# Performance work log

Measured on AMD Instinct MI355X. Metric: run time of the kernel, lower is better.

Reference implementation:

```python
import jax, jax.numpy as jnp
import numpy as np

N = 50000       # nodes
E = 800000      # edges (avg degree 16)
DIN = 64        # input feature dim
HID = 128       # hidden dim (= per-head out_channels in GATConv)
HEADS = 4
G = 64          # graphs in the batch
NC = 8          # num classes
EPS = 1e-5      # BatchNorm eps
NEG_SLOPE = 0.2 # GAT leaky_relu slope


def setup_inputs():
    key = jax.random.key(0)
    it = iter(jax.random.split(key, 40))
    def p(shape, s=0.05):
        return jax.random.normal(next(it), shape, jnp.float32) * s
    x = jax.random.normal(next(it), (N, DIN), jnp.float32)
    edge_index = jax.random.randint(next(it), (2, E), 0, N)
    batch = jnp.sort(jax.random.randint(next(it), (N,), 0, G))
    inp = dict(x=x, edge_index=edge_index, batch=batch)
    inp["s0_Wl"] = p((DIN, HID)); inp["s0_Wr"] = p((DIN, HID)); inp["s0_b"] = p((HID,))
    inp["s1_Wl"] = p((HID, HID)); inp["s1_Wr"] = p((HID, HID)); inp["s1_b"] = p((HID,))
    inp["bn_g"] = 1.0 + p((4, HID)); inp["bn_b"] = p((4, HID))
    inp["bn_m"] = p((4, HID)); inp["bn_v"] = 0.5 + jax.random.uniform(next(it), (4, HID))
    inp["prelu_a"] = 0.25 + p((4, HID))
    for i in range(2):
        inp[f"g{i}_W"] = p((HID, HEADS * HID))
        inp[f"g{i}_as"] = p((HEADS, HID)); inp[f"g{i}_ad"] = p((HEADS, HID))
        inp[f"g{i}_bias"] = p((HID,))
    inp["idp_W"] = p((3, HID, HID)); inp["idp_b"] = p((3, HID)); inp["idp_a"] = 0.25 + p((2, HID))
    inp["cls_W"] = p((HID, NC)); inp["cls_b"] = p((NC,))
    return inp


def _bn(x, g, b, m, v):
    return (x - m) * jax.lax.rsqrt(v + EPS) * g + b


def _prelu(x, a):
    return jnp.where(x >= 0, x, a * x)


def _sage(x, src, dst, Wl, Wr, b):
    # PyG SAGEConv: lin_l(mean_{j->i} x_j) + lin_r(x_i)
    s = jax.ops.segment_sum(x[src], dst, num_segments=N)
    cnt = jax.ops.segment_sum(jnp.ones((src.shape[0],), x.dtype), dst, num_segments=N)
    agg = s / jnp.maximum(cnt, 1.0)[:, None]
    return agg @ Wl + b + x @ Wr


def _gat(x, src, dst, W, a_src, a_dst, bias):
    # src/dst already include self-loops (PyG GATConv default). concat=False -> mean over heads.
    xw = (x @ W).reshape(N, HEADS, HID)               # [N,H,C]
    es = jnp.einsum('nhc,hc->nh', xw, a_src)          # [N,H]
    ed = jnp.einsum('nhc,hc->nh', xw, a_dst)
    e = jax.nn.leaky_relu(es[src] + ed[dst], NEG_SLOPE)   # [E2,H]
    m = jax.lax.stop_gradient(jax.ops.segment_max(e, dst, num_segments=N))
    ex = jnp.exp(e - m[dst])
    den = jax.ops.segment_sum(ex, dst, num_segments=N)
    alpha = ex / den[dst]                                  # [E2,H] softmax per destination
    # per-head scatter to keep peak memory ~[E2,C] instead of [E2,H,C]
    heads = [jax.ops.segment_sum(alpha[:, h:h + 1] * xw[src, h, :], dst, num_segments=N)
             for h in range(HEADS)]
    return jnp.stack(heads, 1).mean(1) + bias


def _model(x, edge_index, batch, s0_Wl, s0_Wr, s0_b, s1_Wl, s1_Wr, s1_b,
           bn_g, bn_b, bn_m, bn_v, prelu_a,
           g0_W, g0_as, g0_ad, g0_bias, g1_W, g1_as, g1_ad, g1_bias,
           idp_W, idp_b, idp_a, cls_W, cls_b):
    src, dst = edge_index[0], edge_index[1]
    h = _sage(x, src, dst, s0_Wl, s0_Wr, s0_b)
    h = _prelu(_bn(h, bn_g[0], bn_b[0], bn_m[0], bn_v[0]), prelu_a[0])
    h = _sage(h, src, dst, s1_Wl, s1_Wr, s1_b)
    h = _prelu(_bn(h, bn_g[1], bn_b[1], bn_m[1], bn_v[1]), prelu_a[1])
    loop = jnp.arange(N)
    src2 = jnp.concatenate([src, loop]); dst2 = jnp.concatenate([dst, loop])
    h = _gat(h, src2, dst2, g0_W, g0_as, g0_ad, g0_bias)
    h = _prelu(_bn(h, bn_g[2], bn_b[2], bn_m[2], bn_v[2]), prelu_a[2])
    h = _gat(h, src2, dst2, g1_W, g1_as, g1_ad, g1_bias)
    h = _prelu(_bn(h, bn_g[3], bn_b[3], bn_m[3], bn_v[3]), prelu_a[3])
    # IDP MLP (dropout inactive in eval)
    h = _prelu(h @ idp_W[0] + idp_b[0], idp_a[0])
    h = _prelu(h @ idp_W[1] + idp_b[1], idp_a[1])
    h = h @ idp_W[2] + idp_b[2]
    # global mean pool per graph
    sums = jax.ops.segment_sum(h, batch, num_segments=G)
    cnt = jax.ops.segment_sum(jnp.ones((N,), h.dtype), batch, num_segments=G)
    gemb = sums / jnp.maximum(cnt, 1.0)[:, None]
    return gemb @ cls_W + cls_b


def reference(x, edge_index, batch, s0_Wl, s0_Wr, s0_b, s1_Wl, s1_Wr, s1_b,
              bn_g, bn_b, bn_m, bn_v, prelu_a,
              g0_W, g0_as, g0_ad, g0_bias, g1_W, g1_as, g1_ad, g1_bias,
              idp_W, idp_b, idp_a, cls_W, cls_b):
    return _model(x, edge_index, batch, s0_Wl, s0_Wr, s0_b, s1_Wl, s1_Wr, s1_b,
                  bn_g, bn_b, bn_m, bn_v, prelu_a,
                  g0_W, g0_as, g0_ad, g0_bias, g1_W, g1_as, g1_ad, g1_bias,
                  idp_W, idp_b, idp_a, cls_W, cls_b)
```

## Files before the change

kernel.cpp:

```cpp
#include <hip/hip_runtime.h>
#include <hip/hip_bf16.h>
#include <math.h>

#define N_NODES 50000
#define N_EDGES 800000
#define DIN     64
#define HID     128
#define HEADS   4
#define NGRAPH  64
#define NCLS    8
#define EPSB    1e-5f
#define SLOPE   0.2f
#define MAXC4   64
#define FP8S    16.0f
#define FP8SI   (0.25f / FP8S)

#define SCB     256
#define NSB     ((N_NODES + SCB - 1) / SCB)

#define MPAD    (N_NODES + 64)
#define TPAD    136

typedef __hip_bfloat16 bf16;
typedef __attribute__((ext_vector_type(8))) short short8;
typedef __attribute__((ext_vector_type(4))) float f32x4;
typedef __attribute__((ext_vector_type(2))) float f32x2;

__device__ __forceinline__ float b2f(bf16 v) { return __bfloat162float(v); }
__device__ __forceinline__ bf16  f2b(float v) { return __float2bfloat16(v); }
__device__ __forceinline__ float lo_f(unsigned v) {
    unsigned u = v << 16; return __builtin_bit_cast(float, u);
}
__device__ __forceinline__ float hi_f(unsigned v) {
    unsigned u = v & 0xffff0000u; return __builtin_bit_cast(float, u);
}
__device__ __forceinline__ unsigned packbf(float lo, float hi) {
    unsigned l = (unsigned)__builtin_bit_cast(unsigned short, __float2bfloat16(lo));
    unsigned h = (unsigned)__builtin_bit_cast(unsigned short, __float2bfloat16(hi));
    return (h << 16) | l;
}

#define PREP_W  229376
#define PREP_X  (N_NODES * DIN)
#define PREP_T  (PREP_W + PREP_X + N_EDGES)
__global__ void k_prep(const float* __restrict__ s0Wl, const float* __restrict__ s0Wr,
                       const float* __restrict__ s1Wl, const float* __restrict__ s1Wr,
                       const float* __restrict__ g0W,  const float* __restrict__ g1W,
                       const float* __restrict__ idpW, const float* __restrict__ x,
                       const int* __restrict__ ei,     const int* __restrict__ batch,
                       bf16* __restrict__ s0t, bf16* __restrict__ s1t,
                       bf16* __restrict__ g0t, bf16* __restrict__ g1t,
                       bf16* __restrict__ idpt, bf16* __restrict__ xbf,
                       int* __restrict__ deg, int* __restrict__ gstart) {
    int t = blockIdx.x * 256 + threadIdx.x;
    if (t < 16384) { int n = t >> 7, k = t & 127;
        s0t[t] = f2b(k < 64 ? s0Wl[k * 128 + n] : s0Wr[(k - 64) * 128 + n]); return; }
    t -= 16384;
    if (t < 32768) { int n = t >> 8, k = t & 255;
        s1t[t] = f2b(k < 128 ? s1Wl[k * 128 + n] : s1Wr[(k - 128) * 128 + n]); return; }
    t -= 32768;
    if (t < 65536) { int n = t >> 7, k = t & 127; g0t[t] = f2b(g0W[k * 512 + n]); return; }
    t -= 65536;
    if (t < 65536) { int n = t >> 7, k = t & 127; g1t[t] = f2b(g1W[k * 512 + n]); return; }
    t -= 65536;
    if (t < 49152) { int l = t >> 14, r = t & 16383; int n = r >> 7, k = r & 127;
        idpt[t] = f2b(idpW[l * 16384 + k * 128 + n]); return; }
    t -= 49152;
    if (t < PREP_X) { xbf[t] = f2b(x[t]); return; }
    t -= PREP_X;
    if (t < N_EDGES) {
        atomicAdd(&deg[ei[N_EDGES + t]], 1);
        int i = t;
        if (i < N_NODES) {
            int b = batch[i];
            int prev = (i == 0) ? -1 : batch[i - 1];
            for (int g = prev + 1; g <= b; ++g) gstart[g] = i;
            if (i == N_NODES - 1)
                for (int g = b + 1; g <= NGRAPH; ++g) gstart[g] = N_NODES;
        }
    }
}

__global__ void k_scan1(const int* __restrict__ deg, int* __restrict__ row_off,
                        int* __restrict__ bsum) {
    __shared__ int sm[SCB];
    int b = blockIdx.x, t = threadIdx.x;
    int i = b * SCB + t;
    int v = (i < N_NODES) ? deg[i] : 0;
    sm[t] = v;
    __syncthreads();
    for (int off = 1; off < SCB; off <<= 1) {
        int x = (t >= off) ? sm[t - off] : 0;
        __syncthreads();
        sm[t] += x;
        __syncthreads();
    }
    if (i < N_NODES) row_off[i + 1] = sm[t];
    if (t == SCB - 1) bsum[b] = sm[t];
}

__global__ void k_scan2(const int* __restrict__ bsum, int* __restrict__ boff) {
    __shared__ int sm[SCB];
    int t = threadIdx.x;
    int v = (t < NSB) ? bsum[t] : 0;
    sm[t] = v;
    __syncthreads();
    for (int off = 1; off < SCB; off <<= 1) {
        int x = (t >= off) ? sm[t - off] : 0;
        __syncthreads();
        sm[t] += x;
        __syncthreads();
    }
    boff[t] = sm[t] - v;
}

__global__ void k_scan3(int* __restrict__ row_off, const int* __restrict__ boff) {
    int i = blockIdx.x * 256 + threadIdx.x;
    if (i == 0) row_off[0] = 0;
    if (i < N_NODES) row_off[i + 1] += boff[i >> 8];
}

__global__ void k_fill(const int* __restrict__ ei, const int* __restrict__ row_off,
                       int* __restrict__ cursor, int* __restrict__ col) {
    int e = blockIdx.x * 256 + threadIdx.x;
    if (e < N_EDGES) {
        int s = ei[e], d = ei[N_EDGES + e];
        int pos = atomicAdd(&cursor[d], 1);
        col[row_off[d] + pos] = s;
    }
}

__global__ __launch_bounds__(256) void k_sage_agg0(
        const bf16* __restrict__ xbf, const float* __restrict__ x,
        const int* __restrict__ row_off, const int* __restrict__ col,
        bf16* __restrict__ acat) {
    __shared__ int sCol[4][MAXC4];
    int w = threadIdx.x >> 6, lane = threadIdx.x & 63;
    int i = blockIdx.x * 4 + w;
    int s0 = row_off[i], s1 = row_off[i + 1];
    const char* xs = (const char*)xbf;
    unsigned loff = (unsigned)lane << 1;
    float acc = 0.f;
    for (int c0 = s0; c0 < s1; c0 += MAXC4) {
        int cnt = min(MAXC4, s1 - c0);
        if (lane < cnt) sCol[w][lane] = col[c0 + lane];
        for (int e = 0; e < cnt; ++e) {
            unsigned off = ((unsigned)sCol[w][e] << 7) | loff;
            acc += lo_f((unsigned)*(const unsigned short*)(xs + off));
        }
    }
    acat[(size_t)i * (2 * DIN) + lane]       = f2b(acc / fmaxf((float)(s1 - s0), 1.0f));
    acat[(size_t)i * (2 * DIN) + DIN + lane] = f2b(x[(size_t)i * DIN + lane]);
}

__global__ __launch_bounds__(256) void k_sage_agg1(
        const unsigned char* __restrict__ hA8, const bf16* __restrict__ hA,
        const int* __restrict__ row_off, const int* __restrict__ col,
        bf16* __restrict__ acat) {
    __shared__ int sCol[4][MAXC4];
    int w = threadIdx.x >> 6, lane = threadIdx.x & 63;
    int i = blockIdx.x * 4 + w;
    int s0 = row_off[i], s1 = row_off[i + 1];
    const char* h8 = (const char*)hA8;
    unsigned loff = (unsigned)lane << 1;
    f32x2 acc = {0.f, 0.f};
    for (int c0 = s0; c0 < s1; c0 += MAXC4) {
        int cnt = min(MAXC4, s1 - c0);
        if (lane < cnt) sCol[w][lane] = col[c0 + lane];
        for (int e = 0; e < cnt; ++e) {
            unsigned off = ((unsigned)sCol[w][e] << 7) | loff;
            f32x2 p = __builtin_amdgcn_cvt_pk_f32_fp8(
                (int)(unsigned)*(const unsigned short*)(h8 + off), false);
            acc += p;
        }
    }
    float inv = 1.0f / (fmaxf((float)(s1 - s0), 1.0f) * FP8S);
    unsigned* ao = (unsigned*)acat;
    ao[(size_t)i * HID + lane]             = packbf(acc.x * inv, acc.y * inv);
    ao[(size_t)i * HID + (HID / 2) + lane] = ((const unsigned*)hA)[(size_t)i * (HID / 2) + lane];
}

template <int K, int NT, int EPI>
__global__ __launch_bounds__(256) void k_gemm(
        const bf16* __restrict__ A, const bf16* __restrict__ Bt, void* __restrict__ Cp,
        unsigned char* __restrict__ C8s, int M, int Nc,
        const float* __restrict__ bias, const float* __restrict__ bng,
        const float* __restrict__ bnb,  const float* __restrict__ bnm,
        const float* __restrict__ bnv,  const float* __restrict__ pa,
        const float* __restrict__ asrc, const float* __restrict__ adst,
        float* __restrict__ es, float* __restrict__ ed) {
    int wave = threadIdx.x >> 6, lane = threadIdx.x & 63;
    int ln = lane & 15, q = lane >> 4;
    int m0 = blockIdx.x * 64 + wave * 16;
    int n0 = blockIdx.y * (NT * 16);
    const bf16* arow = A + (size_t)(m0 + ln) * K + q * 8;

    f32x4 acc[NT];
#pragma unroll
    for (int t = 0; t < NT; ++t) acc[t] = (f32x4){0.f, 0.f, 0.f, 0.f};

#pragma unroll
    for (int k = 0; k < K; k += 32) {
        short8 a = *(const short8*)(const void*)(arow + k);
#pragma unroll
        for (int t = 0; t < NT; ++t) {
            short8 b = *(const short8*)(const void*)(Bt + (size_t)(n0 + t * 16 + ln) * K + k + q * 8);
            acc[t] = __builtin_amdgcn_mfma_f32_16x16x32_bf16(a, b, acc[t], 0, 0, 0);
        }
    }

    if (EPI != 4) {
        bf16* C = (bf16*)Cp;
#pragma unroll
        for (int t = 0; t < NT; ++t) {
            int cidx = n0 + t * 16 + ln;
            float bi = bias[cidx];
            float g = bng[cidx], bb = bnb[cidx], mm = bnm[cidx];
            float iv = rsqrtf(bnv[cidx] + EPSB), al = pa[cidx];
#pragma unroll
            for (int r = 0; r < 4; ++r) {
                int mr = m0 + q * 4 + r;
                if (mr < M) {
                    float v = acc[t][r] + bi;
                    v = (v - mm) * iv * g + bb;
                    v = v >= 0.f ? v : al * v;
                    C[(size_t)mr * Nc + cidx] = f2b(v);
                    if (EPI == 5) {
                        int enc = __builtin_amdgcn_cvt_pk_fp8_f32(v * FP8S, 0.f, 0, false);
                        C8s[(size_t)mr * HID + cidx] = (unsigned char)(enc & 0xff);
                    }
                }
            }
        }
    } else {
        unsigned char* C8 = (unsigned char*)Cp;
#pragma unroll
        for (int t = 0; t < NT; ++t) {
            int cidx = n0 + t * 16 + ln;
#pragma unroll
            for (int r = 0; r < 4; ++r) {
                int mr = m0 + q * 4 + r;
                if (mr < M) {
                    int enc = __builtin_amdgcn_cvt_pk_fp8_f32(acc[t][r] * FP8S, 0.f, 0, false);
                    C8[(size_t)mr * 512 + cidx] = (unsigned char)(enc & 0xff);
                }
            }
        }
        int head = blockIdx.y;
        float asv[NT], adv[NT];
#pragma unroll
        for (int t = 0; t < NT; ++t) {
            asv[t] = asrc[head * HID + t * 16 + ln];
            adv[t] = adst[head * HID + t * 16 + ln];
        }
#pragma unroll
        for (int r = 0; r < 4; ++r) {
            float ps = 0.f, pd = 0.f;
#pragma unroll
            for (int t = 0; t < NT; ++t) { ps += acc[t][r] * asv[t]; pd += acc[t][r] * adv[t]; }
#pragma unroll
            for (int off = 1; off < 16; off <<= 1) {
                ps += __shfl_xor(ps, off, 16);
                pd += __shfl_xor(pd, off, 16);
            }
            int mr = m0 + q * 4 + r;
            if (ln == 0 && mr < M) {
                es[mr * HEADS + head] = ps;
                ed[mr * HEADS + head] = pd;
            }
        }
    }
}

__global__ __launch_bounds__(256) void k_mlp3(
        const bf16* __restrict__ A,
        const bf16* __restrict__ W0t, const bf16* __restrict__ W1t,
        const bf16* __restrict__ W2t,
        const float* __restrict__ b0, const float* __restrict__ a0,
        const float* __restrict__ b1, const float* __restrict__ a1,
        const float* __restrict__ b2,
        bf16* __restrict__ outp, int M) {
    __shared__ bf16 tile[4][16][TPAD];
    int wave = threadIdx.x >> 6, lane = threadIdx.x & 63;
    int ln = lane & 15, q = lane >> 4;
    int m0 = blockIdx.x * 64 + wave * 16;
    bf16* myt = &tile[wave][0][0];

    f32x4 acc[8];
#pragma unroll
    for (int t = 0; t < 8; ++t) acc[t] = (f32x4){0.f, 0.f, 0.f, 0.f};
    {
        const bf16* arow = A + (size_t)(m0 + ln) * HID + q * 8;
#pragma unroll
        for (int k = 0; k < HID; k += 32) {
            short8 a = *(const short8*)(const void*)(arow + k);
#pragma unroll
            for (int t = 0; t < 8; ++t) {
                short8 b = *(const short8*)(const void*)(W0t + (size_t)(t * 16 + ln) * HID + k + q * 8);
                acc[t] = __builtin_amdgcn_mfma_f32_16x16x32_bf16(a, b, acc[t], 0, 0, 0);
            }
        }
#pragma unroll
        for (int t = 0; t < 8; ++t) {
            int c = t * 16 + ln;
            float bi = b0[c], al = a0[c];
#pragma unroll
            for (int r = 0; r < 4; ++r) {
                float v = acc[t][r] + bi;
                v = v >= 0.f ? v : al * v;
                myt[(q * 4 + r) * TPAD + c] = f2b(v);
            }
        }
    }
    {
#pragma unroll
        for (int t = 0; t < 8; ++t) acc[t] = (f32x4){0.f, 0.f, 0.f, 0.f};
#pragma unroll
        for (int k = 0; k < HID; k += 32) {
            short8 a = *(const short8*)(const void*)(&myt[ln * TPAD + k + q * 8]);
#pragma unroll
            for (int t = 0; t < 8; ++t) {
                short8 b = *(const short8*)(const void*)(W1t + (size_t)(t * 16 + ln) * HID + k + q * 8);
                acc[t] = __builtin_amdgcn_mfma_f32_16x16x32_bf16(a, b, acc[t], 0, 0, 0);
            }
        }
#pragma unroll
        for (int t = 0; t < 8; ++t) {
            int c = t * 16 + ln;
            float bi = b1[c], al = a1[c];
#pragma unroll
            for (int r = 0; r < 4; ++r) {
                float v = acc[t][r] + bi;
                v = v >= 0.f ? v : al * v;
                myt[(q * 4 + r) * TPAD + c] = f2b(v);
            }
        }
    }
    {
#pragma unroll
        for (int t = 0; t < 8; ++t) acc[t] = (f32x4){0.f, 0.f, 0.f, 0.f};
#pragma unroll
        for (int k = 0; k < HID; k += 32) {
            short8 a = *(const short8*)(const void*)(&myt[ln * TPAD + k + q * 8]);
#pragma unroll
            for (int t = 0; t < 8; ++t) {
                short8 b = *(const short8*)(const void*)(W2t + (size_t)(t * 16 + ln) * HID + k + q * 8);
                acc[t] = __builtin_amdgcn_mfma_f32_16x16x32_bf16(a, b, acc[t], 0, 0, 0);
            }
        }
#pragma unroll
        for (int t = 0; t < 8; ++t) {
            int c = t * 16 + ln;
            float bi = b2[c];
#pragma unroll
            for (int r = 0; r < 4; ++r) {
                int mr = m0 + q * 4 + r;
                if (mr < M) outp[(size_t)mr * HID + c] = f2b(acc[t][r] + bi);
            }
        }
    }
}

__global__ __launch_bounds__(256) void k_gat_agg(
        const unsigned char* __restrict__ xw8, const float* __restrict__ es,
        const float* __restrict__ ed, const int* __restrict__ row_off,
        const int* __restrict__ col, const float* __restrict__ bias,
        const float* __restrict__ bng, const float* __restrict__ bnb,
        const float* __restrict__ bnm, const float* __restrict__ bnv,
        const float* __restrict__ pa,
        bf16* __restrict__ out) {
    __shared__ __align__(16) float sEx[4][MAXC4][HEADS];
    __shared__ int sCol[4][MAXC4];
    int w = threadIdx.x >> 6;
    int lane = threadIdx.x & 63;
    int i = blockIdx.x * 4 + w;
    int h = lane >> 4;
    const char* esb = (const char*)es;
    unsigned loff = (unsigned)lane << 3;
    float4 edi = ((const float4*)ed)[i];

    int s0 = row_off[i], s1 = row_off[i + 1];
    float den0 = 0.f, den1 = 0.f, den2 = 0.f, den3 = 0.f;
    f32x2 a01 = {0.f, 0.f}, a23 = {0.f, 0.f}, a45 = {0.f, 0.f}, a67 = {0.f, 0.f};

    {
        float4 ev = *(const float4*)(esb + ((unsigned)i << 4));
        float e0 = ev.x + edi.x; e0 = e0 >= 0.f ? e0 : SLOPE * e0; float x0 = expf(e0);
        float e1 = ev.y + edi.y; e1 = e1 >= 0.f ? e1 : SLOPE * e1; float x1 = expf(e1);
        float e2 = ev.z + edi.z; e2 = e2 >= 0.f ? e2 : SLOPE * e2; float x2 = expf(e2);
        float e3 = ev.w + edi.w; e3 = e3 >= 0.f ? e3 : SLOPE * e3; float x3 = expf(e3);
        if (lane == 0) { den0 = x0; den1 = x1; den2 = x2; den3 = x3; }
        float ex = h == 0 ? x0 : h == 1 ? x1 : h == 2 ? x2 : x3;
        f32x2 ex2 = {ex, ex};
        uint2 v = *(const uint2*)(xw8 + (((unsigned)i << 9) | loff));
        a01 = __builtin_elementwise_fma(__builtin_amdgcn_cvt_pk_f32_fp8((int)v.x, false), ex2, a01);
        a23 = __builtin_elementwise_fma(__builtin_amdgcn_cvt_pk_f32_fp8((int)v.x, true),  ex2, a23);
        a45 = __builtin_elementwise_fma(__builtin_amdgcn_cvt_pk_f32_fp8((int)v.y, false), ex2, a45);
        a67 = __builtin_elementwise_fma(__builtin_amdgcn_cvt_pk_f32_fp8((int)v.y, true),  ex2, a67);
    }
    for (int c0 = s0; c0 < s1; c0 += MAXC4) {
        int cnt = min(MAXC4, s1 - c0);
        if (lane < cnt) {
            int sn = col[c0 + lane];
            float4 ev = *(const float4*)(esb + ((unsigned)sn << 4));
            float e0 = ev.x + edi.x; e0 = e0 >= 0.f ? e0 : SLOPE * e0; float x0 = expf(e0);
            float e1 = ev.y + edi.y; e1 = e1 >= 0.f ? e1 : SLOPE * e1; float x1 = expf(e1);
            float e2 = ev.z + edi.z; e2 = e2 >= 0.f ? e2 : SLOPE * e2; float x2 = expf(e2);
            float e3 = ev.w + edi.w; e3 = e3 >= 0.f ? e3 : SLOPE * e3; float x3 = expf(e3);
            den0 += x0; den1 += x1; den2 += x2; den3 += x3;
            sCol[w][lane] = sn;
            f32x4 xv = {x0, x1, x2, x3};
            *(f32x4*)(&sEx[w][lane][0]) = xv;
        }
        for (int e = 0; e < cnt; ++e) {
            float ex = sEx[w][e][h];
            f32x2 ex2 = {ex, ex};
            unsigned off = ((unsigned)sCol[w][e] << 9) | loff;
            uint2 v = *(const uint2*)(xw8 + off);
            a01 = __builtin_elementwise_fma(__builtin_amdgcn_cvt_pk_f32_fp8((int)v.x, false), ex2, a01);
            a23 = __builtin_elementwise_fma(__builtin_amdgcn_cvt_pk_f32_fp8((int)v.x, true),  ex2, a23);
            a45 = __builtin_elementwise_fma(__builtin_amdgcn_cvt_pk_f32_fp8((int)v.y, false), ex2, a45);
            a67 = __builtin_elementwise_fma(__builtin_amdgcn_cvt_pk_f32_fp8((int)v.y, true),  ex2, a67);
        }
    }
    for (int off = 1; off < 64; off <<= 1) {
        den0 += __shfl_xor(den0, off, 64);
        den1 += __shfl_xor(den1, off, 64);
        den2 += __shfl_xor(den2, off, 64);
        den3 += __shfl_xor(den3, off, 64);
    }
    float den = h == 0 ? den0 : h == 1 ? den1 : h == 2 ? den2 : den3;
    float inv = 1.0f / den;
    float m[8] = {a01.x * inv, a01.y * inv, a23.x * inv, a23.y * inv,
                  a45.x * inv, a45.y * inv, a67.x * inv, a67.y * inv};
#pragma unroll
    for (int j = 0; j < 8; ++j) {
        m[j] += __shfl_xor(m[j], 16, 64);
        m[j] += __shfl_xor(m[j], 32, 64);
    }
    if (lane < 16) {
        int cb = lane * 8;
        float r[8];
#pragma unroll
        for (int j = 0; j < 8; ++j) {
            int c = cb + j;
            float v = FP8SI * m[j] + bias[c];
            v = (v - bnm[c]) * rsqrtf(bnv[c] + EPSB) * bng[c] + bnb[c];
            float al = pa[c];
            r[j] = v >= 0.f ? v : al * v;
        }
        uint4 o;
        o.x = packbf(r[0], r[1]); o.y = packbf(r[2], r[3]);
        o.z = packbf(r[4], r[5]); o.w = packbf(r[6], r[7]);
        ((uint4*)out)[(size_t)i * 16 + lane] = o;
    }
}

__global__ __launch_bounds__(256) void k_poolcls(
        const bf16* __restrict__ h, const int* __restrict__ gstart,
        const float* __restrict__ W, const float* __restrict__ b,
        float* __restrict__ out) {
    __shared__ float sO[4][HID];
    __shared__ float gemb[HID];
    int g = blockIdx.x;
    int w = threadIdx.x >> 6, lane = threadIdx.x & 63;
    int b0 = gstart[g], b1 = gstart[g + 1];
    const unsigned* hb = (const unsigned*)h;
    float a0 = 0.f, a1 = 0.f;
    for (int r = b0 + w; r < b1; r += 4) {
        unsigned v = hb[(size_t)r * (HID / 2) + lane];
        a0 += lo_f(v); a1 += hi_f(v);
    }
    sO[w][2 * lane]     = a0;
    sO[w][2 * lane + 1] = a1;
    __syncthreads();
    int t = threadIdx.x;
    if (t < HID) {
        float s = sO[0][t] + sO[1][t] + sO[2][t] + sO[3][t];
        gemb[t] = s / fmaxf((float)(b1 - b0), 1.0f);
    }
    __syncthreads();
    if (t < NCLS) {
        float acc = b[t];
        for (int k = 0; k < HID; ++k) acc += gemb[k] * W[k * NCLS + t];
        out[g * NCLS + t] = acc;
    }
}

extern "C" void kernel_launch(void* const* d_in, const int* in_sizes, int n_in,
                              void* d_out, int out_size, void* d_ws, size_t ws_size,
                              hipStream_t stream) {
    const float* x      = (const float*)d_in[0];
    const int*   ei     = (const int*)d_in[1];
    const int*   batch  = (const int*)d_in[2];
    const float* s0_Wl  = (const float*)d_in[3];
    const float* s0_Wr  = (const float*)d_in[4];
    const float* s0_b   = (const float*)d_in[5];
    const float* s1_Wl  = (const float*)d_in[6];
    const float* s1_Wr  = (const float*)d_in[7];
    const float* s1_b   = (const float*)d_in[8];
    const float* bn_g   = (const float*)d_in[9];
    const float* bn_b   = (const float*)d_in[10];
    const float* bn_m   = (const float*)d_in[11];
    const float* bn_v   = (const float*)d_in[12];
    const float* pre_a  = (const float*)d_in[13];
    const float* g0_W   = (const float*)d_in[14];
    const float* g0_as  = (const float*)d_in[15];
    const float* g0_ad  = (const float*)d_in[16];
    const float* g0_bias= (const float*)d_in[17];
    const float* g1_W   = (const float*)d_in[18];
    const float* g1_as  = (const float*)d_in[19];
    const float* g1_ad  = (const float*)d_in[20];
    const float* g1_bias= (const float*)d_in[21];
    const float* idp_W  = (const float*)d_in[22];
    const float* idp_b  = (const float*)d_in[23];
    const float* idp_a  = (const float*)d_in[24];
    const float* cls_W  = (const float*)d_in[25];
    const float* cls_b  = (const float*)d_in[26];
    float* out = (float*)d_out;

    char* p = (char*)d_ws;
    auto alloc = [&](size_t bytes) -> void* {
        void* r = (void*)p;
        p += (bytes + 255) & ~(size_t)255;
        return r;
    };
    int*   degcur  = (int*)alloc((size_t)2 * N_NODES * 4);
    int*   deg     = degcur;
    int*   cursor  = degcur + N_NODES;
    int*   row_off = (int*)alloc((size_t)(N_NODES + 1) * 4);
    int*   col     = (int*)alloc((size_t)N_EDGES * 4);
    int*   gstart  = (int*)alloc((size_t)(NGRAPH + 1) * 4);
    int*   bsum    = (int*)alloc((size_t)SCB * 4);
    int*   boff    = (int*)alloc((size_t)SCB * 4);
    float* es      = (float*)alloc((size_t)N_NODES * HEADS * 4);
    float* edv     = (float*)alloc((size_t)N_NODES * HEADS * 4);
    bf16*  hA      = (bf16*)alloc((size_t)MPAD * HID * 2);
    bf16*  hB      = (bf16*)alloc((size_t)MPAD * HID * 2);
    bf16*  xbf     = (bf16*)alloc((size_t)N_NODES * DIN * 2);
    unsigned char* hA8 = (unsigned char*)alloc((size_t)MPAD * HID);
    void*  u       = alloc((size_t)MPAD * 512);
    bf16*  acat0   = (bf16*)u;
    bf16*  acat1   = (bf16*)u;
    unsigned char* xw8 = (unsigned char*)u;
    bf16*  s0t     = (bf16*)alloc((size_t)128 * 128 * 2);
    bf16*  s1t     = (bf16*)alloc((size_t)128 * 256 * 2);
    bf16*  g0t     = (bf16*)alloc((size_t)512 * 128 * 2);
    bf16*  g1t     = (bf16*)alloc((size_t)512 * 128 * 2);
    bf16*  idpt    = (bf16*)alloc((size_t)3 * 128 * 128 * 2);

    hipMemsetAsync(degcur, 0, (size_t)2 * N_NODES * 4, stream);

    k_prep<<<(PREP_T + 255) / 256, 256, 0, stream>>>(
        s0_Wl, s0_Wr, s1_Wl, s1_Wr, g0_W, g1_W, idp_W, x, ei, batch,
        s0t, s1t, g0t, g1t, idpt, xbf, deg, gstart);
    k_scan1<<<NSB, SCB, 0, stream>>>(deg, row_off, bsum);
    k_scan2<<<1, SCB, 0, stream>>>(bsum, boff);
    k_scan3<<<(N_NODES + 255) / 256, 256, 0, stream>>>(row_off, boff);
    k_fill<<<(N_EDGES + 255) / 256, 256, 0, stream>>>(ei, row_off, cursor, col);

    const int MB = (N_NODES + 63) / 64;

    k_sage_agg0<<<N_NODES / 4, 256, 0, stream>>>(xbf, x, row_off, col, acat0);
    k_gemm<128, 8, 5><<<dim3(MB, 1), 256, 0, stream>>>(
        acat0, s0t, hA, hA8, N_NODES, HID,
        s0_b, bn_g + 0 * HID, bn_b + 0 * HID, bn_m + 0 * HID, bn_v + 0 * HID, pre_a + 0 * HID,
        nullptr, nullptr, nullptr, nullptr);

    k_sage_agg1<<<N_NODES / 4, 256, 0, stream>>>(hA8, hA, row_off, col, acat1);
    k_gemm<256, 8, 1><<<dim3(MB, 1), 256, 0, stream>>>(
        acat1, s1t, hB, nullptr, N_NODES, HID,
        s1_b, bn_g + 1 * HID, bn_b + 1 * HID, bn_m + 1 * HID, bn_v + 1 * HID, pre_a + 1 * HID,
        nullptr, nullptr, nullptr, nullptr);

    k_gemm<128, 8, 4><<<dim3(MB, 4), 256, 0, stream>>>(
        hB, g0t, xw8, nullptr, N_NODES, HEADS * HID,
        nullptr, nullptr, nullptr, nullptr, nullptr, nullptr,
        g0_as, g0_ad, es, edv);
    k_gat_agg<<<N_NODES / 4, 256, 0, stream>>>(
        xw8, es, edv, row_off, col, g0_bias,
        bn_g + 2 * HID, bn_b + 2 * HID, bn_m + 2 * HID, bn_v + 2 * HID, pre_a + 2 * HID, hA);

    k_gemm<128, 8, 4><<<dim3(MB, 4), 256, 0, stream>>>(
        hA, g1t, xw8, nullptr, N_NODES, HEADS * HID,
        nullptr, nullptr, nullptr, nullptr, nullptr, nullptr,
        g1_as, g1_ad, es, edv);
    k_gat_agg<<<N_NODES / 4, 256, 0, stream>>>(
        xw8, es, edv, row_off, col, g1_bias,
        bn_g + 3 * HID, bn_b + 3 * HID, bn_m + 3 * HID, bn_v + 3 * HID, pre_a + 3 * HID, hB);

    k_mlp3<<<MB, 256, 0, stream>>>(
        hB, idpt + 0 * 16384, idpt + 1 * 16384, idpt + 2 * 16384,
        idp_b + 0 * HID, idp_a + 0 * HID,
        idp_b + 1 * HID, idp_a + 1 * HID,
        idp_b + 2 * HID, hA, N_NODES);

    k_poolcls<<<NGRAPH, 256, 0, stream>>>(hA, gstart, cls_W, cls_b, out);
}
```

Before: 696.8 us.

## Fuse mean-pool into MLP epilogue and gather SAGE layer-0 inputs as FP8

The final MLP kernel now keeps its output tile in shared memory and accumulates per-graph sums directly into a float pool buffer with atomics, using the sorted batch ids. This removes the bf16 write and re-read of the full hidden matrix and replaces the pooling kernel with a tiny classifier kernel. Separately, the input features used for layer-0 neighbor aggregation are stored as scaled FP8 instead of bf16, which halves gather bytes but adds quantization error. The pooling now sums bf16-rounded values through float atomics, so the summation order is no longer deterministic.

```diff
diff --git a/kernel.cpp b/kernel.cpp
--- a/kernel.cpp
+++ b/kernel.cpp
@@ -50,7 +50,7 @@
                        const int* __restrict__ ei,     const int* __restrict__ batch,
                        bf16* __restrict__ s0t, bf16* __restrict__ s1t,
                        bf16* __restrict__ g0t, bf16* __restrict__ g1t,
-                       bf16* __restrict__ idpt, bf16* __restrict__ xbf,
+                       bf16* __restrict__ idpt, unsigned char* __restrict__ x8,
                        int* __restrict__ deg, int* __restrict__ gstart) {
     int t = blockIdx.x * 256 + threadIdx.x;
     if (t < 16384) { int n = t >> 7, k = t & 127;
@@ -66,7 +66,11 @@
     if (t < 49152) { int l = t >> 14, r = t & 16383; int n = r >> 7, k = r & 127;
         idpt[t] = f2b(idpW[l * 16384 + k * 128 + n]); return; }
     t -= 49152;
-    if (t < PREP_X) { xbf[t] = f2b(x[t]); return; }
+    if (t < PREP_X) {
+        int enc = __builtin_amdgcn_cvt_pk_fp8_f32(x[t] * FP8S, 0.f, 0, false);
+        x8[t] = (unsigned char)(enc & 0xff);
+        return;
+    }
     t -= PREP_X;
     if (t < N_EDGES) {
         atomicAdd(&deg[ei[N_EDGES + t]], 1);
@@ -131,25 +135,25 @@
 }
 
 __global__ __launch_bounds__(256) void k_sage_agg0(
-        const bf16* __restrict__ xbf, const float* __restrict__ x,
+        const unsigned char* __restrict__ x8, const float* __restrict__ x,
         const int* __restrict__ row_off, const int* __restrict__ col,
         bf16* __restrict__ acat) {
     __shared__ int sCol[4][MAXC4];
     int w = threadIdx.x >> 6, lane = threadIdx.x & 63;
     int i = blockIdx.x * 4 + w;
     int s0 = row_off[i], s1 = row_off[i + 1];
-    const char* xs = (const char*)xbf;
-    unsigned loff = (unsigned)lane << 1;
     float acc = 0.f;
     for (int c0 = s0; c0 < s1; c0 += MAXC4) {
         int cnt = min(MAXC4, s1 - c0);
         if (lane < cnt) sCol[w][lane] = col[c0 + lane];
         for (int e = 0; e < cnt; ++e) {
-            unsigned off = ((unsigned)sCol[w][e] << 7) | loff;
-            acc += lo_f((unsigned)*(const unsigned short*)(xs + off));
-        }
-    }
-    acat[(size_t)i * (2 * DIN) + lane]       = f2b(acc / fmaxf((float)(s1 - s0), 1.0f));
+            unsigned off = ((unsigned)sCol[w][e] << 6) | (unsigned)lane;
+            f32x2 p = __builtin_amdgcn_cvt_pk_f32_fp8((int)(unsigned)x8[off], false);
+            acc += p.x;
+        }
+    }
+    float inv = 1.0f / (fmaxf((float)(s1 - s0), 1.0f) * FP8S);
+    acat[(size_t)i * (2 * DIN) + lane]       = f2b(acc * inv);
     acat[(size_t)i * (2 * DIN) + DIN + lane] = f2b(x[(size_t)i * DIN + lane]);
 }
 
@@ -278,13 +282,15 @@
         const bf16* __restrict__ W2t,
         const float* __restrict__ b0, const float* __restrict__ a0,
         const float* __restrict__ b1, const float* __restrict__ a1,
-        const float* __restrict__ b2,
-        bf16* __restrict__ outp, int M) {
+        const float* __restrict__ b2, const int* __restrict__ batch,
+        float* __restrict__ pool, int M) {
     __shared__ bf16 tile[4][16][TPAD];
+    __shared__ int sB[4][16];
     int wave = threadIdx.x >> 6, lane = threadIdx.x & 63;
     int ln = lane & 15, q = lane >> 4;
     int m0 = blockIdx.x * 64 + wave * 16;
     bf16* myt = &tile[wave][0][0];
+    if (q == 0) sB[wave][ln] = (m0 + ln < M) ? batch[m0 + ln] : -1;
 
     f32x4 acc[8];
 #pragma unroll
@@ -353,11 +359,28 @@
             int c = t * 16 + ln;
             float bi = b2[c];
 #pragma unroll
-            for (int r = 0; r < 4; ++r) {
-                int mr = m0 + q * 4 + r;
-                if (mr < M) outp[(size_t)mr * HID + c] = f2b(acc[t][r] + bi);
-            }
-        }
+            for (int r = 0; r < 4; ++r)
+                myt[(q * 4 + r) * TPAD + c] = f2b(acc[t][r] + bi);
+        }
+    }
+    float pa0 = 0.f, pa1 = 0.f;
+    int curg = -1;
+    for (int j = 0; j < 16; ++j) {
+        int g = sB[wave][j];
+        if (g < 0) continue;
+        if (g != curg) {
+            if (curg >= 0) {
+                atomicAdd(&pool[curg * HID + 2 * lane], pa0);
+                atomicAdd(&pool[curg * HID + 2 * lane + 1], pa1);
+            }
+            curg = g; pa0 = 0.f; pa1 = 0.f;
+        }
+        unsigned v = *(const unsigned*)&myt[j * TPAD + 2 * lane];
+        pa0 += lo_f(v); pa1 += hi_f(v);
+    }
+    if (curg >= 0) {
+        atomicAdd(&pool[curg * HID + 2 * lane], pa0);
+        atomicAdd(&pool[curg * HID + 2 * lane + 1], pa1);
     }
 }
 
@@ -456,35 +479,16 @@
     }
 }
 
-__global__ __launch_bounds__(256) void k_poolcls(
-        const bf16* __restrict__ h, const int* __restrict__ gstart,
-        const float* __restrict__ W, const float* __restrict__ b,
-        float* __restrict__ out) {
-    __shared__ float sO[4][HID];
-    __shared__ float gemb[HID];
-    int g = blockIdx.x;
-    int w = threadIdx.x >> 6, lane = threadIdx.x & 63;
-    int b0 = gstart[g], b1 = gstart[g + 1];
-    const unsigned* hb = (const unsigned*)h;
-    float a0 = 0.f, a1 = 0.f;
-    for (int r = b0 + w; r < b1; r += 4) {
-        unsigned v = hb[(size_t)r * (HID / 2) + lane];
-        a0 += lo_f(v); a1 += hi_f(v);
-    }
-    sO[w][2 * lane]     = a0;
-    sO[w][2 * lane + 1] = a1;
-    __syncthreads();
+__global__ void k_cls(const float* __restrict__ pool, const int* __restrict__ gstart,
+                      const float* __restrict__ W, const float* __restrict__ b,
+                      float* __restrict__ out) {
     int t = threadIdx.x;
-    if (t < HID) {
-        float s = sO[0][t] + sO[1][t] + sO[2][t] + sO[3][t];
-        gemb[t] = s / fmaxf((float)(b1 - b0), 1.0f);
-    }
-    __syncthreads();
-    if (t < NCLS) {
-        float acc = b[t];
-        for (int k = 0; k < HID; ++k) acc += gemb[k] * W[k * NCLS + t];
-        out[g * NCLS + t] = acc;
-    }
+    int g = t / NCLS, n = t % NCLS;
+    float ic = 1.0f / fmaxf((float)(gstart[g + 1] - gstart[g]), 1.0f);
+    float acc = b[n];
+    for (int k = 0; k < HID; ++k)
+        acc += pool[g * HID + k] * ic * W[k * NCLS + n];
+    out[g * NCLS + n] = acc;
 }
 
 extern "C" void kernel_launch(void* const* d_in, const int* in_sizes, int n_in,
@@ -525,9 +529,10 @@
         p += (bytes + 255) & ~(size_t)255;
         return r;
     };
-    int*   degcur  = (int*)alloc((size_t)2 * N_NODES * 4);
-    int*   deg     = degcur;
-    int*   cursor  = degcur + N_NODES;
+    int*   zb      = (int*)alloc((size_t)(2 * N_NODES + NGRAPH * HID) * 4);
+    int*   deg     = zb;
+    int*   cursor  = zb + N_NODES;
+    float* pool    = (float*)(zb + 2 * N_NODES);
     int*   row_off = (int*)alloc((size_t)(N_NODES + 1) * 4);
     int*   col     = (int*)alloc((size_t)N_EDGES * 4);
     int*   gstart  = (int*)alloc((size_t)(NGRAPH + 1) * 4);
@@ -537,7 +542,7 @@
     float* edv     = (float*)alloc((size_t)N_NODES * HEADS * 4);
     bf16*  hA      = (bf16*)alloc((size_t)MPAD * HID * 2);
     bf16*  hB      = (bf16*)alloc((size_t)MPAD * HID * 2);
-    bf16*  xbf     = (bf16*)alloc((size_t)N_NODES * DIN * 2);
+    unsigned char* x8  = (unsigned char*)alloc((size_t)N_NODES * DIN);
     unsigned char* hA8 = (unsigned char*)alloc((size_t)MPAD * HID);
     void*  u       = alloc((size_t)MPAD * 512);
     bf16*  acat0   = (bf16*)u;
@@ -549,11 +554,11 @@
     bf16*  g1t     = (bf16*)alloc((size_t)512 * 128 * 2);
     bf16*  idpt    = (bf16*)alloc((size_t)3 * 128 * 128 * 2);
 
-    hipMemsetAsync(degcur, 0, (size_t)2 * N_NODES * 4, stream);
+    hipMemsetAsync(zb, 0, (size_t)(2 * N_NODES + NGRAPH * HID) * 4, stream);
 
     k_prep<<<(PREP_T + 255) / 256, 256, 0, stream>>>(
         s0_Wl, s0_Wr, s1_Wl, s1_Wr, g0_W, g1_W, idp_W, x, ei, batch,
-        s0t, s1t, g0t, g1t, idpt, xbf, deg, gstart);
+        s0t, s1t, g0t, g1t, idpt, x8, deg, gstart);
     k_scan1<<<NSB, SCB, 0, stream>>>(deg, row_off, bsum);
     k_scan2<<<1, SCB, 0, stream>>>(bsum, boff);
     k_scan3<<<(N_NODES + 255) / 256, 256, 0, stream>>>(row_off, boff);
@@ -561,7 +566,7 @@
 
     const int MB = (N_NODES + 63) / 64;
 
-    k_sage_agg0<<<N_NODES / 4, 256, 0, stream>>>(xbf, x, row_off, col, acat0);
+    k_sage_agg0<<<N_NODES / 4, 256, 0, stream>>>(x8, x, row_off, col, acat0);
     k_gemm<128, 8, 5><<<dim3(MB, 1), 256, 0, stream>>>(
         acat0, s0t, hA, hA8, N_NODES, HID,
         s0_b, bn_g + 0 * HID, bn_b + 0 * HID, bn_m + 0 * HID, bn_v + 0 * HID, pre_a + 0 * HID,
@@ -593,7 +598,7 @@
         hB, idpt + 0 * 16384, idpt + 1 * 16384, idpt + 2 * 16384,
         idp_b + 0 * HID, idp_a + 0 * HID,
         idp_b + 1 * HID, idp_a + 1 * HID,
-        idp_b + 2 * HID, hA, N_NODES);
-
-    k_poolcls<<<NGRAPH, 256, 0, stream>>>(hA, gstart, cls_W, cls_b, out);
-}
+        idp_b + 2 * HID, batch, pool, N_NODES);
+
+    k_cls<<<1, NGRAPH * NCLS, 0, stream>>>(pool, gstart, cls_W, cls_b, out);
+}
```

New measurement: 629.8 us. 9.6% less time.
